# Kernel optimization log

Measured on AMD Instinct MI355X. Metric: run time of the kernel, lower is better.

Reference implementation:

```python
import jax, jax.numpy as jnp
import numpy as np

N_NODES = 50000; N_INTRA = 800000; N_INTER = 400000; N_IEDGE = 600000
N_GRAPHS = 128; F_IN = 54; DIM = 128; N_GNN = 3; DIM_MLP = 128
DEV_VDW_COEFF = 0.2; EPS_LO = 0.0178; EPS_HI = 0.2
VDW_N_SHORT = 10.0; VDW_N_LONG = 6.0
RANGE_LO = 0.5; RANGE_HI = 5.0
HBOND_CUT = (-0.7, 0.0); METAL_CUT = (-0.7, 0.0); HYDRO_CUT = (0.5, 1.5)


def _lin(key, fi, fo):
    return jax.random.normal(key, (fi, fo), jnp.float32) / np.float32(np.sqrt(fi))


def setup_inputs():
    key = jax.random.key(0)
    ks = iter(jax.random.split(key, 48))
    nk = lambda: next(ks)
    inp = {}
    inp['x'] = jax.random.normal(nk(), (N_NODES, F_IN), jnp.float32)
    inp['pos'] = jax.random.uniform(nk(), (N_NODES, 3), jnp.float32, 0.0, 20.0)
    inp['vdw_radii'] = jax.random.uniform(nk(), (N_NODES,), jnp.float32, 1.0, 2.0)
    inp['rotor'] = jax.random.randint(nk(), (N_GRAPHS, 1), 0, 20).astype(jnp.float32)
    inp['edge_index'] = jax.random.randint(nk(), (2, N_INTRA), 0, N_NODES)
    inp['edge_index_c'] = jax.random.randint(nk(), (2, N_INTER), 0, N_NODES)
    inp['edge_index_i'] = jax.random.randint(nk(), (2, N_IEDGE), 0, N_NODES)
    inp['batch'] = jnp.sort(jax.random.randint(nk(), (N_NODES,), 0, N_GRAPHS))
    for name, p in (('is_metal', 0.02), ('is_h_donor', 0.15), ('is_h_acceptor', 0.2), ('is_hydrophobic', 0.4)):
        inp[name] = jax.random.bernoulli(nk(), p, (N_NODES,))
    inp['embed_W'] = _lin(nk(), F_IN, DIM)
    inp['gat_W'] = jax.random.normal(nk(), (N_GNN, DIM, DIM), jnp.float32) / np.float32(np.sqrt(DIM))
    inp['gat_Wb'] = jnp.zeros((N_GNN, DIM), jnp.float32)
    inp['gat_A'] = 0.1 * jax.random.normal(nk(), (N_GNN, DIM, DIM), jnp.float32) / np.float32(np.sqrt(DIM))
    inp['gat_gate_w'] = jax.random.normal(nk(), (N_GNN, 2 * DIM, 1), jnp.float32) / np.float32(np.sqrt(2 * DIM))
    inp['gat_gate_b'] = jnp.zeros((N_GNN, 1), jnp.float32)
    inp['inter_W'] = jax.random.normal(nk(), (N_GNN, DIM, DIM), jnp.float32) / np.float32(np.sqrt(DIM))
    inp['inter_Wb'] = jnp.zeros((N_GNN, DIM), jnp.float32)
    inp['inter_gate_w'] = jax.random.normal(nk(), (N_GNN, 2 * DIM, 1), jnp.float32) / np.float32(np.sqrt(2 * DIM))
    inp['inter_gate_b'] = jnp.zeros((N_GNN, 1), jnp.float32)
    inp['eps_w1'] = _lin(nk(), 2 * DIM, DIM_MLP); inp['eps_b1'] = jnp.zeros((DIM_MLP,), jnp.float32)
    inp['eps_w2'] = _lin(nk(), DIM_MLP, 1); inp['eps_b2'] = jnp.zeros((1,), jnp.float32)
    inp['dvdw_w1'] = _lin(nk(), 2 * DIM, DIM_MLP); inp['dvdw_b1'] = jnp.zeros((DIM_MLP,), jnp.float32)
    inp['dvdw_w2'] = _lin(nk(), DIM_MLP, 1); inp['dvdw_b2'] = jnp.zeros((1,), jnp.float32)
    inp['hbond_coeff'] = jnp.array([1.0], jnp.float32)
    inp['hydrophobic_coeff'] = jnp.array([0.5], jnp.float32)
    inp['rotor_coeff'] = jnp.array([0.5], jnp.float32)
    return inp


def _gated_gat(x, src, dst, W, Wb, A, gw, gb):
    n = x.shape[0]
    h = x @ W + Wb                                   # [N, D]
    logits = jnp.sum((h @ A)[dst] * h[src], axis=-1)  # per-edge attention logit
    mx = jax.ops.segment_max(logits, dst, num_segments=n)
    mx = jnp.where(jnp.isfinite(mx), mx, 0.0)
    ex = jnp.exp(logits - mx[dst])
    den = jax.ops.segment_sum(ex, dst, num_segments=n)
    alpha = ex / (den[dst] + 1e-16)                  # segment softmax over incoming edges
    h_prime = jax.nn.relu(jax.ops.segment_sum(alpha[:, None] * h[src], dst, num_segments=n))
    z = jax.nn.sigmoid(jnp.concatenate([x, h_prime], -1) @ gw + gb)
    return z * x + (1.0 - z) * h_prime


def _interaction(x, src, dst, W, Wb, gw, gb):
    n = x.shape[0]
    m = jax.ops.segment_sum(jax.nn.relu(x[src] @ W + Wb), dst, num_segments=n)
    z = jax.nn.sigmoid(jnp.concatenate([x, m], -1) @ gw + gb)
    return z * x + (1.0 - z) * m


def _lj(D, R, eps, n_short, n_long):
    dr = jnp.maximum(D / R, 0.5)  # numerical clamp mirroring PIGNet's distance clamp
    n = jnp.where(dr < 1.0, n_short, n_long)
    return eps * (dr ** (-2.0 * n) - 2.0 * dr ** (-n))


def _linear_potential(D, R, minima, c_short, c_long):
    frac = jnp.clip(((D - R) - c_long) / (c_short - c_long), 0.0, 1.0)
    return minima * frac


def _forward(x, pos, vdw_radii, rotor, embed_W, gat_W, gat_Wb, gat_A, gat_gate_w, gat_gate_b,
             inter_W, inter_Wb, inter_gate_w, inter_gate_b,
             eps_w1, eps_b1, eps_w2, eps_b2, dvdw_w1, dvdw_b1, dvdw_w2, dvdw_b2,
             hbond_coeff, hydrophobic_coeff, rotor_coeff,
             edge_index, edge_index_c, edge_index_i, batch,
             is_metal, is_h_donor, is_h_acceptor, is_hydrophobic):
    h = x @ embed_W
    for l in range(N_GNN):
        h = _gated_gat(h, edge_index[0], edge_index[1], gat_W[l], gat_Wb[l], gat_A[l], gat_gate_w[l], gat_gate_b[l])
    for l in range(N_GNN):
        h = _interaction(h, edge_index_c[0], edge_index_c[1], inter_W[l], inter_Wb[l], inter_gate_w[l], inter_gate_b[l])
    i, j = edge_index_i[0], edge_index_i[1]
    diff = pos[i] - pos[j]
    D = jnp.sqrt(jnp.sum(diff * diff, axis=-1) + 1e-10)           # [E]
    rmask = ((D >= RANGE_LO) & (D <= RANGE_HI)).astype(h.dtype)
    x_cat = jnp.concatenate([h[i], h[j]], axis=-1)                # [E, 2*DIM]
    dvdw = jnp.tanh(jax.nn.relu(x_cat @ dvdw_w1 + dvdw_b1) @ dvdw_w2 + dvdw_b2)[:, 0]
    dvdw = dvdw * DEV_VDW_COEFF * rmask
    R = vdw_radii[i] + vdw_radii[j] + dvdw
    eps = jax.nn.sigmoid(jax.nn.relu(x_cat @ eps_w1 + eps_b1) @ eps_w2 + eps_b2)[:, 0]
    eps = eps * (EPS_HI - EPS_LO) + EPS_LO
    min_hb = -hbond_coeff ** 2
    min_hp = -hydrophobic_coeff ** 2
    e = jnp.stack([
        _lj(D, R, eps, VDW_N_SHORT, VDW_N_LONG),
        _linear_potential(D, R, min_hb, *HBOND_CUT),
        _linear_potential(D, R, min_hb, *METAL_CUT),
        _linear_potential(D, R, min_hp, *HYDRO_CUT),
    ])                                                            # [4, E]
    no_metal = ~(is_metal[i] | is_metal[j])
    masks = jnp.stack([
        no_metal,
        ((is_h_donor[i] & is_h_acceptor[j]) | (is_h_acceptor[i] & is_h_donor[j])) & no_metal,
        (is_metal[i] & is_h_acceptor[j]) | (is_h_acceptor[i] & is_metal[j]),
        is_hydrophobic[i] & is_hydrophobic[j] & no_metal,
    ]).astype(e.dtype)
    e = e * masks * rmask
    energies = jax.ops.segment_sum(e.T, batch[i], num_segments=N_GRAPHS)  # [G, 4]
    penalty = 1.0 + rotor_coeff ** 2 * rotor                               # [G, 1]
    return energies / penalty, dvdw


def reference(x, pos, vdw_radii, rotor, edge_index, edge_index_c, edge_index_i, batch,
              is_metal, is_h_donor, is_h_acceptor, is_hydrophobic,
              embed_W, gat_W, gat_Wb, gat_A, gat_gate_w, gat_gate_b,
              inter_W, inter_Wb, inter_gate_w, inter_gate_b,
              eps_w1, eps_b1, eps_w2, eps_b2, dvdw_w1, dvdw_b1, dvdw_w2, dvdw_b2,
              hbond_coeff, hydrophobic_coeff, rotor_coeff):
    return _forward(x, pos, vdw_radii, rotor, embed_W, gat_W, gat_Wb, gat_A, gat_gate_w, gat_gate_b,
                    inter_W, inter_Wb, inter_gate_w, inter_gate_b,
                    eps_w1, eps_b1, eps_w2, eps_b2, dvdw_w1, dvdw_b1, dvdw_w2, dvdw_b2,
                    hbond_coeff, hydrophobic_coeff, rotor_coeff,
                    edge_index, edge_index_c, edge_index_i, batch,
                    is_metal, is_h_donor, is_h_acceptor, is_hydrophobic)
```

## Files before the change

### kernel.cpp

```cpp
#include <hip/hip_runtime.h>
#include <math.h>

#define NN 50000
#define EA 800000
#define EC 400000
#define EIN 600000
#define NG 128
#define FIN 54

#define DEV_VDW 0.2f
#define EPS_LO_ 0.0178f
#define EPS_HI_ 0.2f

typedef unsigned int uint;
typedef unsigned short ushort;
typedef __attribute__((ext_vector_type(8))) short bf16x8;
typedef __attribute__((ext_vector_type(4))) float f32x4;

__device__ __forceinline__ ushort f2bf(float f){
  uint x = __float_as_uint(f);
  uint r = x + 0x7fffu + ((x >> 16) & 1u);
  return (ushort)(r >> 16);
}
__device__ __forceinline__ uint f2bf2(float a, float b){
  return (uint)f2bf(a) | ((uint)f2bf(b) << 16);
}
__device__ __forceinline__ void decode8(uint4 u, float* f){
  f[0] = __uint_as_float(u.x << 16); f[1] = __uint_as_float(u.x & 0xffff0000u);
  f[2] = __uint_as_float(u.y << 16); f[3] = __uint_as_float(u.y & 0xffff0000u);
  f[4] = __uint_as_float(u.z << 16); f[5] = __uint_as_float(u.z & 0xffff0000u);
  f[6] = __uint_as_float(u.w << 16); f[7] = __uint_as_float(u.w & 0xffff0000u);
}

__global__ void k_count3(const int* __restrict__ dstA, const int* __restrict__ dstC,
                         const int* __restrict__ dstI,
                         int* __restrict__ cntA, int* __restrict__ cntC, int* __restrict__ cntI){
  int b = blockIdx.x;
  const int* dst; int* cnt; int E; int bid; int nb;
  if (b < 1024){ dst = dstA; cnt = cntA; E = EA;  bid = b;        nb = 1024; }
  else if (b < 1536){ dst = dstC; cnt = cntC; E = EC;  bid = b - 1024; nb = 512; }
  else { dst = dstI; cnt = cntI; E = EIN; bid = b - 1536; nb = 1024; }
  for (int i = bid * 256 + threadIdx.x; i < E; i += nb * 256) atomicAdd(&cnt[dst[i]], 1);
}

__global__ void k_scan3(const int* __restrict__ cntA, int* __restrict__ offA, int* __restrict__ curA,
                        const int* __restrict__ cntC, int* __restrict__ offC, int* __restrict__ curC,
                        const int* __restrict__ cntI, int* __restrict__ offI, int* __restrict__ curI){
  const int* cnt = (blockIdx.x == 0) ? cntA : (blockIdx.x == 1) ? cntC : cntI;
  int* off = (blockIdx.x == 0) ? offA : (blockIdx.x == 1) ? offC : offI;
  int* cur = (blockIdx.x == 0) ? curA : (blockIdx.x == 1) ? curC : curI;
  int n = NN;
  __shared__ int wsums[16];
  __shared__ int run_s;
  int tid = threadIdx.x;
  int lane = tid & 63, w = tid >> 6;
  if (tid == 0) run_s = 0;
  __syncthreads();
  for (int base = 0; base < n; base += 1024){
    int run = run_s;
    int i = base + tid;
    int v = (i < n) ? cnt[i] : 0;
    int s = v;
    #pragma unroll
    for (int o = 1; o < 64; o <<= 1){ int t = __shfl_up(s, o, 64); if (lane >= o) s += t; }
    if (lane == 63) wsums[w] = s;
    __syncthreads();
    if (w == 0 && lane < 16){
      int t = wsums[lane];
      #pragma unroll
      for (int o = 1; o < 16; o <<= 1){ int u = __shfl_up(t, o, 64); if (lane >= o) t += u; }
      wsums[lane] = t;
    }
    __syncthreads();
    int woff = (w == 0) ? 0 : wsums[w - 1];
    int excl = run + woff + (s - v);
    if (i < n){ off[i] = excl; cur[i] = excl; }
    int tot = wsums[15];
    __syncthreads();
    if (tid == 0) run_s = run + tot;
    __syncthreads();
  }
  if (threadIdx.x == 0) off[n] = run_s;
}

__global__ void k_place3(const int* __restrict__ eiA, const int* __restrict__ eiC,
                         const int* __restrict__ eiI,
                         int* __restrict__ curA, int* __restrict__ srcA,
                         int* __restrict__ curC, int* __restrict__ srcC,
                         int* __restrict__ curI, int* __restrict__ srcI, int* __restrict__ eidI){
  int b = blockIdx.x;
  if (b < 1024){
    for (int i = b * 256 + threadIdx.x; i < EA; i += 1024 * 256){
      int d = eiA[EA + i];
      int slot = atomicAdd(&curA[d], 1);
      srcA[slot] = eiA[i];
    }
  } else if (b < 1536){
    int bid = b - 1024;
    for (int i = bid * 256 + threadIdx.x; i < EC; i += 512 * 256){
      int d = eiC[EC + i];
      int slot = atomicAdd(&curC[d], 1);
      srcC[slot] = eiC[i];
    }
  } else {
    int bid = b - 1536;
    for (int i = bid * 256 + threadIdx.x; i < EIN; i += 1024 * 256){
      int key = eiI[i];
      int slot = atomicAdd(&curI[key], 1);
      srcI[slot] = eiI[EIN + i];
      eidI[slot] = i;
    }
  }
}

__global__ void k_nodeinfo(const float* __restrict__ POS, const float* __restrict__ RAD,
                           const int* __restrict__ Mmet, const int* __restrict__ Mdon,
                           const int* __restrict__ Macc, const int* __restrict__ Mhyd,
                           const int* __restrict__ BATCH,
                           float4* __restrict__ PRAD, uint* __restrict__ MB){
  int n = blockIdx.x * 256 + threadIdx.x;
  if (n < NN){
    PRAD[n] = make_float4(POS[3*n], POS[3*n+1], POS[3*n+2], RAD[n]);
    uint m = (Mmet[n] ? 1u : 0u) | (Mdon[n] ? 2u : 0u) | (Macc[n] ? 4u : 0u) |
             (Mhyd[n] ? 8u : 0u) | ((uint)BATCH[n] << 8);
    MB[n] = m;
  }
}

__global__ __launch_bounds__(256) void k_prepw(const float* __restrict__ gatW, const float* __restrict__ gatA,
                        const float* __restrict__ intW, const float* __restrict__ dw1,
                        const float* __restrict__ ew1,
                        const float* __restrict__ gatWb, const float* __restrict__ intWb,
                        const float* __restrict__ db1, const float* __restrict__ eb1,
                        uint* __restrict__ Wt, float* __restrict__ BIASALL){
  __shared__ ushort L[128 * 132];
  int m = blockIdx.x;
  int tid = threadIdx.x;
  if (m == 13){
    for (int idx = tid; idx < 13 * 128; idx += 256){
      int slot = idx >> 7, c = idx & 127;
      if (slot >= 3 && slot < 6) continue;
      float v = 0.f;
      if (slot < 3) v = gatWb[slot * 128 + c];
      else if (slot < 9) v = intWb[(slot - 6) * 128 + c];
      else if (slot == 9) v = db1[c];
      else if (slot == 11) v = eb1[c];
      BIASALL[idx] = v;
    }
    return;
  }
  if (m >= 3 && m < 6){
    int l = m - 3;
    const float* Wf  = gatW + l * 16384;
    const float* Af  = gatA + l * 16384;
    const float* Wbf = gatWb + l * 128;
    for (int idx = tid; idx < 16384; idx += 256){
      int k = idx >> 7, n = idx & 127;
      L[k * 132 + n] = f2bf(Af[idx]);
    }
    __syncthreads();
    int r = tid >> 1, ch = tid & 1;
    float accv[64];
    #pragma unroll
    for (int c = 0; c < 64; ++c) accv[c] = 0.f;
    float accb = 0.f;
    int bc = tid & 127;
    for (int mm = 0; mm < 128; ++mm){
      float wv = Wf[r * 128 + mm];
      const uint* Lr32 = (const uint*)&L[mm * 132 + ch * 64];
      #pragma unroll
      for (int c2 = 0; c2 < 32; ++c2){
        uint u = Lr32[c2];
        accv[2 * c2]     += wv * __uint_as_float(u << 16);
        accv[2 * c2 + 1] += wv * __uint_as_float(u & 0xffff0000u);
      }
      accb += Wbf[mm] * __uint_as_float((uint)L[mm * 132 + bc] << 16);
    }
    __syncthreads();
    #pragma unroll
    for (int c = 0; c < 64; ++c) L[r * 132 + ch * 64 + c] = f2bf(accv[c]);
    if (tid < 128) BIASALL[(3 + l) * 128 + tid] = accb;
    __syncthreads();
    int n = tid & 127, half = tid >> 7;
    uint* outp = Wt + (size_t)m * 8192 + n * 64 + half * 32;
    #pragma unroll
    for (int kk2 = 0; kk2 < 32; ++kk2){
      int k = half * 64 + 2 * kk2;
      uint u = (uint)L[k * 132 + n] | ((uint)L[(k + 1) * 132 + n] << 16);
      outp[kk2] = u;
    }
    return;
  }
  const float* src = (m < 3)  ? gatW + m * 16384 :
                     (m < 9)  ? intW + (m - 6) * 16384 :
                     (m < 11) ? dw1 + (m - 9) * 16384 :
                                ew1 + (m - 11) * 16384;
  for (int idx = tid; idx < 16384; idx += 256){
    int k = idx >> 7, n = idx & 127;
    L[k * 132 + n] = f2bf(src[idx]);
  }
  __syncthreads();
  int n = tid & 127, half = tid >> 7;
  uint* outp = Wt + (size_t)m * 8192 + n * 64 + half * 32;
  #pragma unroll
  for (int kk2 = 0; kk2 < 32; ++kk2){
    int k = half * 64 + 2 * kk2;
    uint u = (uint)L[k * 132 + n] | ((uint)L[(k + 1) * 132 + n] << 16);
    outp[kk2] = u;
  }
}

__global__ void k_embed(const float* __restrict__ X, const float* __restrict__ W,
                        float* __restrict__ H, uint* __restrict__ Hh){
  __shared__ float Wls[FIN * 128];
  int tid = threadIdx.x;
  for (int i = tid; i < FIN * 128; i += 128) Wls[i] = W[i];
  __syncthreads();
  for (int row = blockIdx.x; row < NN; row += gridDim.x){
    const float* xr = X + row * FIN;
    float acc = 0.f;
    #pragma unroll
    for (int k = 0; k < FIN; ++k) acc += xr[k] * Wls[k * 128 + tid];
    H[(size_t)row * 128 + tid] = acc;
    ((ushort*)Hh)[(size_t)row * 128 + tid] = f2bf(acc);
  }
}

template<bool RELU>
__global__ __launch_bounds__(256) void k_gemm_mfma(const uint* __restrict__ Ah,
        const uint* __restrict__ Bt0, size_t strideB,
        const float* __restrict__ bias0, size_t strideBias,
        uint* __restrict__ C0, size_t strideC, int N){
  const uint* Bt = Bt0 + (size_t)blockIdx.y * strideB;
  const float* bias = bias0 + (size_t)blockIdx.y * strideBias;
  uint* Cout = C0 + (size_t)blockIdx.y * strideC;
  int tid = threadIdx.x;
  int lane = tid & 63;
  int wv = tid >> 6;
  int row0 = blockIdx.x * 128 + wv * 32;
  int l15 = lane & 15, lg = lane >> 4;
  int ra0 = row0 + l15, ra1 = row0 + 16 + l15;
  const uint* pa0 = Ah + (size_t)(ra0 < N ? ra0 : 0) * 64 + lg * 4;
  const uint* pa1 = Ah + (size_t)(ra1 < N ? ra1 : 0) * 64 + lg * 4;
  const uint* pb  = Bt + (size_t)l15 * 64 + lg * 4;
  f32x4 acc[2][8] = {};
  #pragma unroll
  for (int c = 0; c < 4; ++c){
    bf16x8 a0 = *(const bf16x8*)(pa0 + c * 16);
    bf16x8 a1 = *(const bf16x8*)(pa1 + c * 16);
    #pragma unroll
    for (int ct = 0; ct < 8; ++ct){
      bf16x8 b = *(const bf16x8*)(pb + ct * 1024 + c * 16);
      acc[0][ct] = __builtin_amdgcn_mfma_f32_16x16x32_bf16(a0, b, acc[0][ct], 0, 0, 0);
      acc[1][ct] = __builtin_amdgcn_mfma_f32_16x16x32_bf16(a1, b, acc[1][ct], 0, 0, 0);
    }
  }
  #pragma unroll
  for (int ct = 0; ct < 8; ++ct){
    int col = ct * 16 + l15;
    float bv = bias[col];
    #pragma unroll
    for (int rt = 0; rt < 2; ++rt){
      int rbase = row0 + rt * 16 + lg * 4;
      f32x4 a4 = acc[rt][ct];
      #pragma unroll
      for (int r = 0; r < 4; ++r){
        int row = rbase + r;
        if (row < N){
          float t = a4[r] + bv;
          if (RELU) t = fmaxf(t, 0.f);
          ((ushort*)Cout)[(size_t)row * 128 + col] = f2bf(t);
        }
      }
    }
  }
}

__global__ __launch_bounds__(256) void k_gat(float* __restrict__ H, uint* __restrict__ Hh,
                      const uint* __restrict__ HWh, const uint* __restrict__ HAh,
                      const int* __restrict__ off, const int* __restrict__ srcs,
                      const float* __restrict__ GW, const float* __restrict__ GB){
  int tid = threadIdx.x;
  int sub = tid & 15;
  int n = blockIdx.x * 16 + (tid >> 4);
  if (n >= NN) return;
  uint4 au = *(const uint4*)(HAh + (size_t)n * 64 + sub * 4);
  float a[8]; decode8(au, a);
  int e0 = off[n], deg = off[n + 1] - e0;
  float m = -INFINITY, den = 0.f;
  float acc[8] = {};
  uint4 w0v = {}, w1v = {};
  if (deg > 0) w0v = *(const uint4*)(HWh + (size_t)srcs[e0] * 64 + sub * 4);
  if (deg > 1) w1v = *(const uint4*)(HWh + (size_t)srcs[e0 + 1] * 64 + sub * 4);
  for (int t = 0; t < deg; ++t){
    uint4 wn = {};
    if (t + 2 < deg) wn = *(const uint4*)(HWh + (size_t)srcs[e0 + t + 2] * 64 + sub * 4);
    float w[8]; decode8(w0v, w);
    float p = a[0]*w[0] + a[1]*w[1] + a[2]*w[2] + a[3]*w[3]
            + a[4]*w[4] + a[5]*w[5] + a[6]*w[6] + a[7]*w[7];
    #pragma unroll
    for (int o = 8; o; o >>= 1) p += __shfl_xor(p, o, 64);
    float mn = fmaxf(m, p);
    float cf = __expf(m - mn);
    float ex = __expf(p - mn);
    den = den * cf + ex;
    #pragma unroll
    for (int q = 0; q < 8; ++q) acc[q] = acc[q] * cf + ex * w[q];
    m = mn;
    w0v = w1v; w1v = wn;
  }
  float inv = 1.f / (den + 1e-16f);
  float hp[8];
  #pragma unroll
  for (int q = 0; q < 8; ++q) hp[q] = fmaxf(acc[q] * inv, 0.f);
  float x[8];
  *(float4*)&x[0] = *(const float4*)(H + (size_t)n * 128 + sub * 8);
  *(float4*)&x[4] = *(const float4*)(H + (size_t)n * 128 + sub * 8 + 4);
  float gx[8], gh[8];
  *(float4*)&gx[0] = *(const float4*)(GW + sub * 8);
  *(float4*)&gx[4] = *(const float4*)(GW + sub * 8 + 4);
  *(float4*)&gh[0] = *(const float4*)(GW + 128 + sub * 8);
  *(float4*)&gh[4] = *(const float4*)(GW + 128 + sub * 8 + 4);
  float g = 0.f;
  #pragma unroll
  for (int q = 0; q < 8; ++q) g += x[q] * gx[q] + hp[q] * gh[q];
  #pragma unroll
  for (int o = 8; o; o >>= 1) g += __shfl_xor(g, o, 64);
  g += GB[0];
  float z = 1.f / (1.f + __expf(-g));
  #pragma unroll
  for (int q = 0; q < 8; ++q) x[q] = z * x[q] + (1.f - z) * hp[q];
  *(float4*)(H + (size_t)n * 128 + sub * 8)     = *(float4*)&x[0];
  *(float4*)(H + (size_t)n * 128 + sub * 8 + 4) = *(float4*)&x[4];
  uint4 hw;
  hw.x = f2bf2(x[0], x[1]); hw.y = f2bf2(x[2], x[3]);
  hw.z = f2bf2(x[4], x[5]); hw.w = f2bf2(x[6], x[7]);
  *(uint4*)(Hh + (size_t)n * 64 + sub * 4) = hw;
}

__global__ __launch_bounds__(256) void k_inter(float* __restrict__ H, uint* __restrict__ Hh,
                        const uint* __restrict__ Th,
                        const int* __restrict__ off, const int* __restrict__ srcs,
                        const float* __restrict__ GW, const float* __restrict__ GB){
  int tid = threadIdx.x;
  int sub = tid & 15;
  int n = blockIdx.x * 16 + (tid >> 4);
  if (n >= NN) return;
  int e0 = off[n], deg = off[n + 1] - e0;
  float acc[8] = {};
  uint4 w0v = {}, w1v = {};
  if (deg > 0) w0v = *(const uint4*)(Th + (size_t)srcs[e0] * 64 + sub * 4);
  if (deg > 1) w1v = *(const uint4*)(Th + (size_t)srcs[e0 + 1] * 64 + sub * 4);
  for (int t = 0; t < deg; ++t){
    uint4 wn = {};
    if (t + 2 < deg) wn = *(const uint4*)(Th + (size_t)srcs[e0 + t + 2] * 64 + sub * 4);
    float w[8]; decode8(w0v, w);
    #pragma unroll
    for (int q = 0; q < 8; ++q) acc[q] += w[q];
    w0v = w1v; w1v = wn;
  }
  float x[8];
  *(float4*)&x[0] = *(const float4*)(H + (size_t)n * 128 + sub * 8);
  *(float4*)&x[4] = *(const float4*)(H + (size_t)n * 128 + sub * 8 + 4);
  float gx[8], gh[8];
  *(float4*)&gx[0] = *(const float4*)(GW + sub * 8);
  *(float4*)&gx[4] = *(const float4*)(GW + sub * 8 + 4);
  *(float4*)&gh[0] = *(const float4*)(GW + 128 + sub * 8);
  *(float4*)&gh[4] = *(const float4*)(GW + 128 + sub * 8 + 4);
  float g = 0.f;
  #pragma unroll
  for (int q = 0; q < 8; ++q) g += x[q] * gx[q] + acc[q] * gh[q];
  #pragma unroll
  for (int o = 8; o; o >>= 1) g += __shfl_xor(g, o, 64);
  g += GB[0];
  float z = 1.f / (1.f + __expf(-g));
  #pragma unroll
  for (int q = 0; q < 8; ++q) x[q] = z * x[q] + (1.f - z) * acc[q];
  *(float4*)(H + (size_t)n * 128 + sub * 8)     = *(float4*)&x[0];
  *(float4*)(H + (size_t)n * 128 + sub * 8 + 4) = *(float4*)&x[4];
  uint4 hw;
  hw.x = f2bf2(x[0], x[1]); hw.y = f2bf2(x[2], x[3]);
  hw.z = f2bf2(x[4], x[5]); hw.w = f2bf2(x[6], x[7]);
  *(uint4*)(Hh + (size_t)n * 64 + sub * 4) = hw;
}

__global__ __launch_bounds__(256) void k_edges(
    const int* __restrict__ offI, const int* __restrict__ srcI, const int* __restrict__ eidI,
    const float4* __restrict__ PRAD, const uint* __restrict__ MB,
    const uint* __restrict__ Pd, const uint* __restrict__ Qd,
    const uint* __restrict__ Pe, const uint* __restrict__ Qe,
    const float* __restrict__ w2d, const float* __restrict__ b2d,
    const float* __restrict__ w2e, const float* __restrict__ b2e,
    const float* __restrict__ hbc, const float* __restrict__ hpc,
    float* __restrict__ geng, float* __restrict__ outdv){
  int tid = threadIdx.x;
  int sub = tid & 15;
  int n = blockIdx.x * 16 + (tid >> 4);
  if (n >= NN) return;
  int e0 = offI[n], deg = offI[n + 1] - e0;
  if (deg == 0) return;
  float wdv[8], wev[8];
  *(float4*)&wdv[0] = *(const float4*)(w2d + sub * 8);
  *(float4*)&wdv[4] = *(const float4*)(w2d + sub * 8 + 4);
  *(float4*)&wev[0] = *(const float4*)(w2e + sub * 8);
  *(float4*)&wev[4] = *(const float4*)(w2e + sub * 8 + 4);
  float bd = b2d[0], be = b2e[0];
  float minhb = -hbc[0] * hbc[0], minhp = -hpc[0] * hpc[0];
  uint4 pdu = *(const uint4*)(Pd + (size_t)n * 64 + sub * 4);
  uint4 peu = *(const uint4*)(Pe + (size_t)n * 64 + sub * 4);
  float pdf[8], pef[8];
  decode8(pdu, pdf); decode8(peu, pef);
  float4 pri = PRAD[n];
  uint mbi = MB[n];
  float E0 = 0.f, E1 = 0.f, E2 = 0.f, E3 = 0.f;

  int ee0 = eidI[e0];
  int j0 = srcI[e0];
  uint4 qd0 = *(const uint4*)(Qd + (size_t)j0 * 64 + sub * 4);
  uint4 qe0 = *(const uint4*)(Qe + (size_t)j0 * 64 + sub * 4);
  float4 prj0 = PRAD[j0];
  uint mbj0 = MB[j0];

  for (int t = 0; t < deg; ++t){
    int ee1 = 0; uint4 qd1 = {}, qe1 = {}; float4 prj1 = {}; uint mbj1 = 0;
    if (t + 1 < deg){
      int j1 = srcI[e0 + t + 1];
      ee1 = eidI[e0 + t + 1];
      qd1 = *(const uint4*)(Qd + (size_t)j1 * 64 + sub * 4);
      qe1 = *(const uint4*)(Qe + (size_t)j1 * 64 + sub * 4);
      prj1 = PRAD[j1]; mbj1 = MB[j1];
    }
    float qdf[8], qef[8];
    decode8(qd0, qdf); decode8(qe0, qef);
    float sd = 0.f, se = 0.f;
    #pragma unroll
    for (int q = 0; q < 8; ++q){
      sd += fmaxf(pdf[q] + qdf[q], 0.f) * wdv[q];
      se += fmaxf(pef[q] + qef[q], 0.f) * wev[q];
    }
    #pragma unroll
    for (int o = 8; o; o >>= 1){
      sd += __shfl_xor(sd, o, 64);
      se += __shfl_xor(se, o, 64);
    }
    sd += bd; se += be;
    float dx = pri.x - prj0.x, dy = pri.y - prj0.y, dz = pri.z - prj0.z;
    float D = sqrtf(dx * dx + dy * dy + dz * dz + 1e-10f);
    float rmask = (D >= 0.5f && D <= 5.0f) ? 1.f : 0.f;
    float ex2 = __expf(2.f * fminf(sd, 15.f));
    float th = __fdividef(ex2 - 1.f, ex2 + 1.f);
    float dvdw = th * DEV_VDW * rmask;
    float eps = __fdividef(1.f, 1.f + __expf(-se)) * (EPS_HI_ - EPS_LO_) + EPS_LO_;
    float R = pri.w + prj0.w + dvdw;
    float dr = fmaxf(__fdividef(D, R), 0.5f);
    float nn2 = (dr < 1.f) ? 10.f : 6.f;
    float tp = __expf(-nn2 * __logf(dr));
    float ev = eps * (tp * tp - 2.f * tp);
    float dmr = D - R;
    float f1 = fminf(fmaxf(dmr * (-1.f / 0.7f), 0.f), 1.f);
    float f3 = fminf(fmaxf(1.5f - dmr, 0.f), 1.f);
    bool metI = mbi & 1, metJ = mbj0 & 1;
    bool donI = mbi & 2, donJ = mbj0 & 2;
    bool accI = mbi & 4, accJ = mbj0 & 4;
    bool hyI  = mbi & 8, hyJ  = mbj0 & 8;
    bool nm = !(metI || metJ);
    if (sub == 0) outdv[ee0] = dvdw;
    E0 += nm ? ev * rmask : 0.f;
    E1 += (((donI && accJ) || (accI && donJ)) && nm) ? minhb * f1 * rmask : 0.f;
    E2 += ((metI && accJ) || (accI && metJ)) ? minhb * f1 * rmask : 0.f;
    E3 += (hyI && hyJ && nm) ? minhp * f3 * rmask : 0.f;
    ee0 = ee1; qd0 = qd1; qe0 = qe1; prj0 = prj1; mbj0 = mbj1;
  }
  if (sub == 0){
    float* part = geng + (size_t)(blockIdx.x & 7) * (NG * 4);
    int g = (int)(mbi >> 8) * 4;
    atomicAdd(&part[g + 0], E0);
    atomicAdd(&part[g + 1], E1);
    atomicAdd(&part[g + 2], E2);
    atomicAdd(&part[g + 3], E3);
  }
}

__global__ void k_final(const float* __restrict__ geng, const float* __restrict__ rotor,
                        const float* __restrict__ rc, float* __restrict__ out){
  int t = blockIdx.x * blockDim.x + threadIdx.x;
  if (t < NG * 4){
    int g = t >> 2;
    float s = 0.f;
    #pragma unroll
    for (int p = 0; p < 8; ++p) s += geng[p * NG * 4 + t];
    float pen = 1.f + rc[0] * rc[0] * rotor[g];
    out[t] = s / pen;
  }
}

extern "C" void kernel_launch(void* const* d_in, const int* in_sizes, int n_in,
                              void* d_out, int out_size, void* d_ws, size_t ws_size,
                              hipStream_t stream){
  (void)in_sizes; (void)n_in; (void)out_size; (void)ws_size;
  const float* X    = (const float*)d_in[0];
  const float* POS  = (const float*)d_in[1];
  const float* RAD  = (const float*)d_in[2];
  const float* ROT  = (const float*)d_in[3];
  const int* EIa    = (const int*)d_in[4];
  const int* EIc    = (const int*)d_in[5];
  const int* EIi    = (const int*)d_in[6];
  const int* BATCH  = (const int*)d_in[7];
  const int* Mmet = (const int*)d_in[8];
  const int* Mdon = (const int*)d_in[9];
  const int* Macc = (const int*)d_in[10];
  const int* Mhyd = (const int*)d_in[11];
  const float* embW  = (const float*)d_in[12];
  const float* gatW  = (const float*)d_in[13];
  const float* gatWb = (const float*)d_in[14];
  const float* gatA  = (const float*)d_in[15];
  const float* gatGw = (const float*)d_in[16];
  const float* gatGb = (const float*)d_in[17];
  const float* intW  = (const float*)d_in[18];
  const float* intWb = (const float*)d_in[19];
  const float* intGw = (const float*)d_in[20];
  const float* intGb = (const float*)d_in[21];
  const float* ew1 = (const float*)d_in[22];
  const float* eb1 = (const float*)d_in[23];
  const float* ew2 = (const float*)d_in[24];
  const float* eb2 = (const float*)d_in[25];
  const float* dw1 = (const float*)d_in[26];
  const float* db1 = (const float*)d_in[27];
  const float* dw2 = (const float*)d_in[28];
  const float* db2 = (const float*)d_in[29];
  const float* hbc = (const float*)d_in[30];
  const float* hpc = (const float*)d_in[31];
  const float* rcc = (const float*)d_in[32];
  float* out = (float*)d_out;

  char* w = (char*)d_ws;
  float* H   = (float*)w; w += (size_t)NN * 128 * 4;
  uint* Hh   = (uint*)w;  w += (size_t)NN * 64 * 4;
  uint* BAh  = (uint*)w;  w += (size_t)NN * 64 * 4;
  uint* BBh  = (uint*)w;  w += (size_t)NN * 64 * 4;
  uint* Peh  = (uint*)w;  w += (size_t)NN * 64 * 4;
  uint* Qeh  = (uint*)w;  w += (size_t)NN * 64 * 4;
  uint* WT   = (uint*)w;  w += (size_t)13 * 8192 * 4;
  float* BIASALL = (float*)w; w += (size_t)13 * 128 * 4;
  float4* PRAD = (float4*)w; w += (size_t)NN * 16;
  uint* MBb  = (uint*)w;  w += (size_t)NN * 4;
  float* GENG = (float*)w; w += (size_t)8 * 512 * 4;
  int* cntA = (int*)w; w += (size_t)NN * 4;
  int* offA = (int*)w; w += (size_t)(NN + 1) * 4;
  int* curA = (int*)w; w += (size_t)NN * 4;
  int* srcA = (int*)w; w += (size_t)EA * 4;
  int* cntC = (int*)w; w += (size_t)NN * 4;
  int* offC = (int*)w; w += (size_t)(NN + 1) * 4;
  int* curC = (int*)w; w += (size_t)NN * 4;
  int* srcC = (int*)w; w += (size_t)EC * 4;
  int* cntI = (int*)w; w += (size_t)NN * 4;
  int* offI = (int*)w; w += (size_t)(NN + 1) * 4;
  int* curI = (int*)w; w += (size_t)NN * 4;
  int* srcI = (int*)w; w += (size_t)EIN * 4;
  int* eidI = (int*)w; w += (size_t)EIN * 4;
  uint* Th  = BAh;
  uint* Pdh = BAh;
  uint* Qdh = BBh;

  hipMemsetAsync(cntA, 0, (size_t)NN * 4, stream);
  hipMemsetAsync(cntC, 0, (size_t)NN * 4, stream);
  hipMemsetAsync(cntI, 0, (size_t)NN * 4, stream);
  hipMemsetAsync(GENG, 0, (size_t)8 * 512 * 4, stream);

  k_count3<<<2560, 256, 0, stream>>>(EIa + EA, EIc + EC, EIi, cntA, cntC, cntI);
  k_scan3<<<3, 1024, 0, stream>>>(cntA, offA, curA, cntC, offC, curC, cntI, offI, curI);
  k_place3<<<2560, 256, 0, stream>>>(EIa, EIc, EIi, curA, srcA, curC, srcC, curI, srcI, eidI);

  k_prepw<<<14, 256, 0, stream>>>(gatW, gatA, intW, dw1, ew1, gatWb, intWb, db1, eb1, WT, BIASALL);
  k_nodeinfo<<<(NN + 255) / 256, 256, 0, stream>>>(POS, RAD, Mmet, Mdon, Macc, Mhyd, BATCH, PRAD, MBb);
  k_embed<<<2048, 128, 0, stream>>>(X, embW, H, Hh);

  int gg = (NN + 127) / 128;
  int nodeGrid = (NN + 15) / 16;
  for (int l = 0; l < 3; ++l){
    k_gemm_mfma<false><<<dim3(gg, 2), 256, 0, stream>>>(Hh, WT + (size_t)l * 8192, (size_t)3 * 8192,
                                                        BIASALL + l * 128, (size_t)3 * 128,
                                                        BAh, (size_t)NN * 64, NN);
    k_gat<<<nodeGrid, 256, 0, stream>>>(H, Hh, BAh, BBh, offA, srcA, gatGw + l * 256, gatGb + l);
  }
  for (int l = 0; l < 3; ++l){
    k_gemm_mfma<true><<<dim3(gg, 1), 256, 0, stream>>>(Hh, WT + (size_t)(6 + l) * 8192, 0,
                                                       BIASALL + (6 + l) * 128, 0, Th, 0, NN);
    k_inter<<<nodeGrid, 256, 0, stream>>>(H, Hh, Th, offC, srcC, intGw + l * 256, intGb + l);
  }
  k_gemm_mfma<false><<<dim3(gg, 4), 256, 0, stream>>>(Hh, WT + (size_t)9 * 8192, (size_t)8192,
                                                      BIASALL + 9 * 128, (size_t)128,
                                                      BAh, (size_t)NN * 64, NN);

  k_edges<<<nodeGrid, 256, 0, stream>>>(offI, srcI, eidI, PRAD, MBb, Pdh, Qdh, Peh, Qeh,
                                        dw2, db2, ew2, eb2, hbc, hpc,
                                        GENG, out + 512);
  k_final<<<2, 256, 0, stream>>>(GENG, ROT, rcc, out);
}
```

Baseline: 991.2 us.

## Rank-based CSR build, drop fp32 node state, deepen gather prefetch, pack edge ids

The CSR build now records each edge's atomic rank while counting, so the place pass writes with non-temporal stores and no second round of atomics. The fp32 node feature array H is removed and the GAT and inter layers read the residual from the bf16 copy, which saves bandwidth but adds bf16 rounding to the residual path. Neighbor gathers in the GAT and inter layers prefetch three rows ahead instead of two. The interaction edge source and edge id are packed into one 64-bit word, and dvdw outputs use non-temporal stores.

```diff
diff --git a/kernel.cpp b/kernel.cpp
--- a/kernel.cpp
+++ b/kernel.cpp
@@ -14,6 +14,7 @@
 
 typedef unsigned int uint;
 typedef unsigned short ushort;
+typedef unsigned long long ull;
 typedef __attribute__((ext_vector_type(8))) short bf16x8;
 typedef __attribute__((ext_vector_type(4))) float f32x4;
 
@@ -32,23 +33,24 @@
   f[6] = __uint_as_float(u.w << 16); f[7] = __uint_as_float(u.w & 0xffff0000u);
 }
 
-__global__ void k_count3(const int* __restrict__ dstA, const int* __restrict__ dstC,
-                         const int* __restrict__ dstI,
-                         int* __restrict__ cntA, int* __restrict__ cntC, int* __restrict__ cntI){
+__global__ void k_rank(const int* __restrict__ dstA, const int* __restrict__ dstC,
+                       const int* __restrict__ dstI,
+                       int* __restrict__ cntA, int* __restrict__ cntC, int* __restrict__ cntI,
+                       int* __restrict__ rnkA, int* __restrict__ rnkC, int* __restrict__ rnkI){
   int b = blockIdx.x;
-  const int* dst; int* cnt; int E; int bid; int nb;
-  if (b < 1024){ dst = dstA; cnt = cntA; E = EA;  bid = b;        nb = 1024; }
-  else if (b < 1536){ dst = dstC; cnt = cntC; E = EC;  bid = b - 1024; nb = 512; }
-  else { dst = dstI; cnt = cntI; E = EIN; bid = b - 1536; nb = 1024; }
-  for (int i = bid * 256 + threadIdx.x; i < E; i += nb * 256) atomicAdd(&cnt[dst[i]], 1);
-}
-
-__global__ void k_scan3(const int* __restrict__ cntA, int* __restrict__ offA, int* __restrict__ curA,
-                        const int* __restrict__ cntC, int* __restrict__ offC, int* __restrict__ curC,
-                        const int* __restrict__ cntI, int* __restrict__ offI, int* __restrict__ curI){
+  const int* dst; int* cnt; int* rnk; int E; int bid; int nb;
+  if (b < 1024){ dst = dstA; cnt = cntA; rnk = rnkA; E = EA;  bid = b;        nb = 1024; }
+  else if (b < 1536){ dst = dstC; cnt = cntC; rnk = rnkC; E = EC;  bid = b - 1024; nb = 512; }
+  else { dst = dstI; cnt = cntI; rnk = rnkI; E = EIN; bid = b - 1536; nb = 1024; }
+  for (int i = bid * 256 + threadIdx.x; i < E; i += nb * 256)
+    rnk[i] = atomicAdd(&cnt[dst[i]], 1);
+}
+
+__global__ void k_scan3(const int* __restrict__ cntA, int* __restrict__ offA,
+                        const int* __restrict__ cntC, int* __restrict__ offC,
+                        const int* __restrict__ cntI, int* __restrict__ offI){
   const int* cnt = (blockIdx.x == 0) ? cntA : (blockIdx.x == 1) ? cntC : cntI;
   int* off = (blockIdx.x == 0) ? offA : (blockIdx.x == 1) ? offC : offI;
-  int* cur = (blockIdx.x == 0) ? curA : (blockIdx.x == 1) ? curC : curI;
   int n = NN;
   __shared__ int wsums[16];
   __shared__ int run_s;
@@ -74,7 +76,7 @@
     __syncthreads();
     int woff = (w == 0) ? 0 : wsums[w - 1];
     int excl = run + woff + (s - v);
-    if (i < n){ off[i] = excl; cur[i] = excl; }
+    if (i < n) off[i] = excl;
     int tot = wsums[15];
     __syncthreads();
     if (tid == 0) run_s = run + tot;
@@ -83,32 +85,29 @@
   if (threadIdx.x == 0) off[n] = run_s;
 }
 
-__global__ void k_place3(const int* __restrict__ eiA, const int* __restrict__ eiC,
-                         const int* __restrict__ eiI,
-                         int* __restrict__ curA, int* __restrict__ srcA,
-                         int* __restrict__ curC, int* __restrict__ srcC,
-                         int* __restrict__ curI, int* __restrict__ srcI, int* __restrict__ eidI){
+__global__ void k_place(const int* __restrict__ eiA, const int* __restrict__ eiC,
+                        const int* __restrict__ eiI,
+                        const int* __restrict__ offA, const int* __restrict__ rnkA, int* __restrict__ srcA,
+                        const int* __restrict__ offC, const int* __restrict__ rnkC, int* __restrict__ srcC,
+                        const int* __restrict__ offI, const int* __restrict__ rnkI, ull* __restrict__ jeI){
   int b = blockIdx.x;
   if (b < 1024){
     for (int i = b * 256 + threadIdx.x; i < EA; i += 1024 * 256){
       int d = eiA[EA + i];
-      int slot = atomicAdd(&curA[d], 1);
-      srcA[slot] = eiA[i];
+      __builtin_nontemporal_store(eiA[i], &srcA[offA[d] + rnkA[i]]);
     }
   } else if (b < 1536){
     int bid = b - 1024;
     for (int i = bid * 256 + threadIdx.x; i < EC; i += 512 * 256){
       int d = eiC[EC + i];
-      int slot = atomicAdd(&curC[d], 1);
-      srcC[slot] = eiC[i];
+      __builtin_nontemporal_store(eiC[i], &srcC[offC[d] + rnkC[i]]);
     }
   } else {
     int bid = b - 1536;
     for (int i = bid * 256 + threadIdx.x; i < EIN; i += 1024 * 256){
       int key = eiI[i];
-      int slot = atomicAdd(&curI[key], 1);
-      srcI[slot] = eiI[EIN + i];
-      eidI[slot] = i;
+      ull v = ((ull)(uint)i << 32) | (uint)eiI[EIN + i];
+      __builtin_nontemporal_store(v, &jeI[offI[key] + rnkI[i]]);
     }
   }
 }
@@ -211,7 +210,7 @@
 }
 
 __global__ void k_embed(const float* __restrict__ X, const float* __restrict__ W,
-                        float* __restrict__ H, uint* __restrict__ Hh){
+                        uint* __restrict__ Hh){
   __shared__ float Wls[FIN * 128];
   int tid = threadIdx.x;
   for (int i = tid; i < FIN * 128; i += 128) Wls[i] = W[i];
@@ -221,7 +220,6 @@
     float acc = 0.f;
     #pragma unroll
     for (int k = 0; k < FIN; ++k) acc += xr[k] * Wls[k * 128 + tid];
-    H[(size_t)row * 128 + tid] = acc;
     ((ushort*)Hh)[(size_t)row * 128 + tid] = f2bf(acc);
   }
 }
@@ -276,7 +274,7 @@
   }
 }
 
-__global__ __launch_bounds__(256) void k_gat(float* __restrict__ H, uint* __restrict__ Hh,
+__global__ __launch_bounds__(256) void k_gat(uint* __restrict__ Hh,
                       const uint* __restrict__ HWh, const uint* __restrict__ HAh,
                       const int* __restrict__ off, const int* __restrict__ srcs,
                       const float* __restrict__ GW, const float* __restrict__ GB){
@@ -289,12 +287,13 @@
   int e0 = off[n], deg = off[n + 1] - e0;
   float m = -INFINITY, den = 0.f;
   float acc[8] = {};
-  uint4 w0v = {}, w1v = {};
+  uint4 w0v = {}, w1v = {}, w2v = {};
   if (deg > 0) w0v = *(const uint4*)(HWh + (size_t)srcs[e0] * 64 + sub * 4);
   if (deg > 1) w1v = *(const uint4*)(HWh + (size_t)srcs[e0 + 1] * 64 + sub * 4);
+  if (deg > 2) w2v = *(const uint4*)(HWh + (size_t)srcs[e0 + 2] * 64 + sub * 4);
   for (int t = 0; t < deg; ++t){
     uint4 wn = {};
-    if (t + 2 < deg) wn = *(const uint4*)(HWh + (size_t)srcs[e0 + t + 2] * 64 + sub * 4);
+    if (t + 3 < deg) wn = *(const uint4*)(HWh + (size_t)srcs[e0 + t + 3] * 64 + sub * 4);
     float w[8]; decode8(w0v, w);
     float p = a[0]*w[0] + a[1]*w[1] + a[2]*w[2] + a[3]*w[3]
             + a[4]*w[4] + a[5]*w[5] + a[6]*w[6] + a[7]*w[7];
@@ -307,15 +306,14 @@
     #pragma unroll
     for (int q = 0; q < 8; ++q) acc[q] = acc[q] * cf + ex * w[q];
     m = mn;
-    w0v = w1v; w1v = wn;
+    w0v = w1v; w1v = w2v; w2v = wn;
   }
   float inv = 1.f / (den + 1e-16f);
   float hp[8];
   #pragma unroll
   for (int q = 0; q < 8; ++q) hp[q] = fmaxf(acc[q] * inv, 0.f);
-  float x[8];
-  *(float4*)&x[0] = *(const float4*)(H + (size_t)n * 128 + sub * 8);
-  *(float4*)&x[4] = *(const float4*)(H + (size_t)n * 128 + sub * 8 + 4);
+  uint4 xu = *(const uint4*)(Hh + (size_t)n * 64 + sub * 4);
+  float x[8]; decode8(xu, x);
   float gx[8], gh[8];
   *(float4*)&gx[0] = *(const float4*)(GW + sub * 8);
   *(float4*)&gx[4] = *(const float4*)(GW + sub * 8 + 4);
@@ -330,15 +328,13 @@
   float z = 1.f / (1.f + __expf(-g));
   #pragma unroll
   for (int q = 0; q < 8; ++q) x[q] = z * x[q] + (1.f - z) * hp[q];
-  *(float4*)(H + (size_t)n * 128 + sub * 8)     = *(float4*)&x[0];
-  *(float4*)(H + (size_t)n * 128 + sub * 8 + 4) = *(float4*)&x[4];
   uint4 hw;
   hw.x = f2bf2(x[0], x[1]); hw.y = f2bf2(x[2], x[3]);
   hw.z = f2bf2(x[4], x[5]); hw.w = f2bf2(x[6], x[7]);
   *(uint4*)(Hh + (size_t)n * 64 + sub * 4) = hw;
 }
 
-__global__ __launch_bounds__(256) void k_inter(float* __restrict__ H, uint* __restrict__ Hh,
+__global__ __launch_bounds__(256) void k_inter(uint* __restrict__ Hh,
                         const uint* __restrict__ Th,
                         const int* __restrict__ off, const int* __restrict__ srcs,
                         const float* __restrict__ GW, const float* __restrict__ GB){
@@ -348,20 +344,20 @@
   if (n >= NN) return;
   int e0 = off[n], deg = off[n + 1] - e0;
   float acc[8] = {};
-  uint4 w0v = {}, w1v = {};
+  uint4 w0v = {}, w1v = {}, w2v = {};
   if (deg > 0) w0v = *(const uint4*)(Th + (size_t)srcs[e0] * 64 + sub * 4);
   if (deg > 1) w1v = *(const uint4*)(Th + (size_t)srcs[e0 + 1] * 64 + sub * 4);
+  if (deg > 2) w2v = *(const uint4*)(Th + (size_t)srcs[e0 + 2] * 64 + sub * 4);
   for (int t = 0; t < deg; ++t){
     uint4 wn = {};
-    if (t + 2 < deg) wn = *(const uint4*)(Th + (size_t)srcs[e0 + t + 2] * 64 + sub * 4);
+    if (t + 3 < deg) wn = *(const uint4*)(Th + (size_t)srcs[e0 + t + 3] * 64 + sub * 4);
     float w[8]; decode8(w0v, w);
     #pragma unroll
     for (int q = 0; q < 8; ++q) acc[q] += w[q];
-    w0v = w1v; w1v = wn;
-  }
-  float x[8];
-  *(float4*)&x[0] = *(const float4*)(H + (size_t)n * 128 + sub * 8);
-  *(float4*)&x[4] = *(const float4*)(H + (size_t)n * 128 + sub * 8 + 4);
+    w0v = w1v; w1v = w2v; w2v = wn;
+  }
+  uint4 xu = *(const uint4*)(Hh + (size_t)n * 64 + sub * 4);
+  float x[8]; decode8(xu, x);
   float gx[8], gh[8];
   *(float4*)&gx[0] = *(const float4*)(GW + sub * 8);
   *(float4*)&gx[4] = *(const float4*)(GW + sub * 8 + 4);
@@ -376,8 +372,6 @@
   float z = 1.f / (1.f + __expf(-g));
   #pragma unroll
   for (int q = 0; q < 8; ++q) x[q] = z * x[q] + (1.f - z) * acc[q];
-  *(float4*)(H + (size_t)n * 128 + sub * 8)     = *(float4*)&x[0];
-  *(float4*)(H + (size_t)n * 128 + sub * 8 + 4) = *(float4*)&x[4];
   uint4 hw;
   hw.x = f2bf2(x[0], x[1]); hw.y = f2bf2(x[2], x[3]);
   hw.z = f2bf2(x[4], x[5]); hw.w = f2bf2(x[6], x[7]);
@@ -385,7 +379,7 @@
 }
 
 __global__ __launch_bounds__(256) void k_edges(
-    const int* __restrict__ offI, const int* __restrict__ srcI, const int* __restrict__ eidI,
+    const int* __restrict__ offI, const ull* __restrict__ jeI,
     const float4* __restrict__ PRAD, const uint* __restrict__ MB,
     const uint* __restrict__ Pd, const uint* __restrict__ Qd,
     const uint* __restrict__ Pe, const uint* __restrict__ Qe,
@@ -414,18 +408,18 @@
   uint mbi = MB[n];
   float E0 = 0.f, E1 = 0.f, E2 = 0.f, E3 = 0.f;
 
-  int ee0 = eidI[e0];
-  int j0 = srcI[e0];
+  ull je0 = jeI[e0];
+  int j0 = (int)(uint)je0;
   uint4 qd0 = *(const uint4*)(Qd + (size_t)j0 * 64 + sub * 4);
   uint4 qe0 = *(const uint4*)(Qe + (size_t)j0 * 64 + sub * 4);
   float4 prj0 = PRAD[j0];
   uint mbj0 = MB[j0];
 
   for (int t = 0; t < deg; ++t){
-    int ee1 = 0; uint4 qd1 = {}, qe1 = {}; float4 prj1 = {}; uint mbj1 = 0;
+    ull je1 = 0; uint4 qd1 = {}, qe1 = {}; float4 prj1 = {}; uint mbj1 = 0;
     if (t + 1 < deg){
-      int j1 = srcI[e0 + t + 1];
-      ee1 = eidI[e0 + t + 1];
+      je1 = jeI[e0 + t + 1];
+      int j1 = (int)(uint)je1;
       qd1 = *(const uint4*)(Qd + (size_t)j1 * 64 + sub * 4);
       qe1 = *(const uint4*)(Qe + (size_t)j1 * 64 + sub * 4);
       prj1 = PRAD[j1]; mbj1 = MB[j1];
@@ -464,12 +458,12 @@
     bool accI = mbi & 4, accJ = mbj0 & 4;
     bool hyI  = mbi & 8, hyJ  = mbj0 & 8;
     bool nm = !(metI || metJ);
-    if (sub == 0) outdv[ee0] = dvdw;
+    if (sub == 0) __builtin_nontemporal_store(dvdw, &outdv[(int)(je0 >> 32)]);
     E0 += nm ? ev * rmask : 0.f;
     E1 += (((donI && accJ) || (accI && donJ)) && nm) ? minhb * f1 * rmask : 0.f;
     E2 += ((metI && accJ) || (accI && metJ)) ? minhb * f1 * rmask : 0.f;
     E3 += (hyI && hyJ && nm) ? minhp * f3 * rmask : 0.f;
-    ee0 = ee1; qd0 = qd1; qe0 = qe1; prj0 = prj1; mbj0 = mbj1;
+    je0 = je1; qd0 = qd1; qe0 = qe1; prj0 = prj1; mbj0 = mbj1;
   }
   if (sub == 0){
     float* part = geng + (size_t)(blockIdx.x & 7) * (NG * 4);
@@ -534,7 +528,6 @@
   float* out = (float*)d_out;
 
   char* w = (char*)d_ws;
-  float* H   = (float*)w; w += (size_t)NN * 128 * 4;
   uint* Hh   = (uint*)w;  w += (size_t)NN * 64 * 4;
   uint* BAh  = (uint*)w;  w += (size_t)NN * 64 * 4;
   uint* BBh  = (uint*)w;  w += (size_t)NN * 64 * 4;
@@ -547,17 +540,16 @@
   float* GENG = (float*)w; w += (size_t)8 * 512 * 4;
   int* cntA = (int*)w; w += (size_t)NN * 4;
   int* offA = (int*)w; w += (size_t)(NN + 1) * 4;
-  int* curA = (int*)w; w += (size_t)NN * 4;
   int* srcA = (int*)w; w += (size_t)EA * 4;
+  int* rnkA = (int*)w; w += (size_t)EA * 4;
   int* cntC = (int*)w; w += (size_t)NN * 4;
   int* offC = (int*)w; w += (size_t)(NN + 1) * 4;
-  int* curC = (int*)w; w += (size_t)NN * 4;
   int* srcC = (int*)w; w += (size_t)EC * 4;
+  int* rnkC = (int*)w; w += (size_t)EC * 4;
   int* cntI = (int*)w; w += (size_t)NN * 4;
   int* offI = (int*)w; w += (size_t)(NN + 1) * 4;
-  int* curI = (int*)w; w += (size_t)NN * 4;
-  int* srcI = (int*)w; w += (size_t)EIN * 4;
-  int* eidI = (int*)w; w += (size_t)EIN * 4;
+  int* rnkI = (int*)w; w += (size_t)EIN * 4;
+  ull* jeI  = (ull*)w; w += (size_t)EIN * 8;
   uint* Th  = BAh;
   uint* Pdh = BAh;
   uint* Qdh = BBh;
@@ -567,13 +559,13 @@
   hipMemsetAsync(cntI, 0, (size_t)NN * 4, stream);
   hipMemsetAsync(GENG, 0, (size_t)8 * 512 * 4, stream);
 
-  k_count3<<<2560, 256, 0, stream>>>(EIa + EA, EIc + EC, EIi, cntA, cntC, cntI);
-  k_scan3<<<3, 1024, 0, stream>>>(cntA, offA, curA, cntC, offC, curC, cntI, offI, curI);
-  k_place3<<<2560, 256, 0, stream>>>(EIa, EIc, EIi, curA, srcA, curC, srcC, curI, srcI, eidI);
+  k_rank<<<2560, 256, 0, stream>>>(EIa + EA, EIc + EC, EIi, cntA, cntC, cntI, rnkA, rnkC, rnkI);
+  k_scan3<<<3, 1024, 0, stream>>>(cntA, offA, cntC, offC, cntI, offI);
+  k_place<<<2560, 256, 0, stream>>>(EIa, EIc, EIi, offA, rnkA, srcA, offC, rnkC, srcC, offI, rnkI, jeI);
 
   k_prepw<<<14, 256, 0, stream>>>(gatW, gatA, intW, dw1, ew1, gatWb, intWb, db1, eb1, WT, BIASALL);
   k_nodeinfo<<<(NN + 255) / 256, 256, 0, stream>>>(POS, RAD, Mmet, Mdon, Macc, Mhyd, BATCH, PRAD, MBb);
-  k_embed<<<2048, 128, 0, stream>>>(X, embW, H, Hh);
+  k_embed<<<2048, 128, 0, stream>>>(X, embW, Hh);
 
   int gg = (NN + 127) / 128;
   int nodeGrid = (NN + 15) / 16;
@@ -581,18 +573,18 @@
     k_gemm_mfma<false><<<dim3(gg, 2), 256, 0, stream>>>(Hh, WT + (size_t)l * 8192, (size_t)3 * 8192,
                                                         BIASALL + l * 128, (size_t)3 * 128,
                                                         BAh, (size_t)NN * 64, NN);
-    k_gat<<<nodeGrid, 256, 0, stream>>>(H, Hh, BAh, BBh, offA, srcA, gatGw + l * 256, gatGb + l);
+    k_gat<<<nodeGrid, 256, 0, stream>>>(Hh, BAh, BBh, offA, srcA, gatGw + l * 256, gatGb + l);
   }
   for (int l = 0; l < 3; ++l){
     k_gemm_mfma<true><<<dim3(gg, 1), 256, 0, stream>>>(Hh, WT + (size_t)(6 + l) * 8192, 0,
                                                        BIASALL + (6 + l) * 128, 0, Th, 0, NN);
-    k_inter<<<nodeGrid, 256, 0, stream>>>(H, Hh, Th, offC, srcC, intGw + l * 256, intGb + l);
+    k_inter<<<nodeGrid, 256, 0, stream>>>(Hh, Th, offC, srcC, intGw + l * 256, intGb + l);
   }
   k_gemm_mfma<false><<<dim3(gg, 4), 256, 0, stream>>>(Hh, WT + (size_t)9 * 8192, (size_t)8192,
                                                       BIASALL + 9 * 128, (size_t)128,
                                                       BAh, (size_t)NN * 64, NN);
 
-  k_edges<<<nodeGrid, 256, 0, stream>>>(offI, srcI, eidI, PRAD, MBb, Pdh, Qdh, Peh, Qeh,
+  k_edges<<<nodeGrid, 256, 0, stream>>>(offI, jeI, PRAD, MBb, Pdh, Qdh, Peh, Qeh,
                                         dw2, db2, ew2, eb2, hbc, hpc,
                                         GENG, out + 512);
   k_final<<<2, 256, 0, stream>>>(GENG, ROT, rcc, out);
```

Measured after the change: 889.0 us. 10.3% less time.
